# Performance work log

Measured on AMD Instinct MI355X. Metric: run time of the kernel, lower is better.

Reference implementation:

```python
import jax, jax.numpy as jnp
import numpy as np

B, T, DM, H, DH, P = 8, 512, 1024, 16, 64, 3584


def rotate_half(x):
    x1, x2 = x[..., : x.shape[-1] // 2], x[..., x.shape[-1] // 2 :]
    return jnp.concatenate([-x2, x1], axis=-1)


def setup_inputs() -> dict:
    key = jax.random.key(0)
    ks = jax.random.split(key, 16)
    x_new = jax.random.normal(ks[0], (B, T, DM), dtype=jnp.float32)
    # realistic RoPE tables for positions [P, P+T)
    inv_freq = 1.0 / (10000.0 ** (jnp.arange(0, DH, 2, dtype=jnp.float32) / DH))
    pos = jnp.arange(P, P + T, dtype=jnp.float32)
    freqs = pos[:, None] * inv_freq[None, :]  # [T, DH/2]
    emb = jnp.concatenate([freqs, freqs], axis=-1)  # [T, DH]
    rotary_cos = jnp.cos(emb)[None, None]  # [1,1,T,DH]
    rotary_sin = jnp.sin(emb)[None, None]
    past_k = jax.random.normal(ks[1], (B, H, P, DH), dtype=jnp.float32)
    past_v = jax.random.normal(ks[2], (B, H, P, DH), dtype=jnp.float32)
    past_lengths = jax.random.randint(ks[3], (B,), 0, P + 1, dtype=jnp.int32)
    new_token_counts = jax.random.randint(ks[4], (B,), 1, T + 1, dtype=jnp.int32)
    valid_new_mask = jnp.arange(T)[None, :] < new_token_counts[:, None]  # [B,T] bool
    s = 0.02
    Wq = jax.random.normal(ks[5], (DM, DM), dtype=jnp.float32) * s
    Wk = jax.random.normal(ks[6], (DM, DM), dtype=jnp.float32) * s
    Wv = jax.random.normal(ks[7], (DM, DM), dtype=jnp.float32) * s
    Wo = jax.random.normal(ks[8], (DM, DM), dtype=jnp.float32) * s
    bq = jax.random.normal(ks[9], (DM,), dtype=jnp.float32) * s
    bk = jax.random.normal(ks[10], (DM,), dtype=jnp.float32) * s
    bv = jax.random.normal(ks[11], (DM,), dtype=jnp.float32) * s
    bo = jax.random.normal(ks[12], (DM,), dtype=jnp.float32) * s
    return dict(x_new=x_new, rotary_cos=rotary_cos, rotary_sin=rotary_sin,
                past_k=past_k, past_v=past_v, past_lengths=past_lengths,
                valid_new_mask=valid_new_mask, new_token_counts=new_token_counts,
                Wq=Wq, bq=bq, Wk=Wk, bk=bk, Wv=Wv, bv=bv, Wo=Wo, bo=bo)


def reference(x_new, rotary_cos, rotary_sin, past_k, past_v, past_lengths,
              valid_new_mask, new_token_counts, Wq, bq, Wk, bk, Wv, bv, Wo, bo):
    b, t, _ = x_new.shape
    # projections -> [B,H,T,DH]
    def proj(W, bias):
        y = x_new @ W + bias
        return y.reshape(b, t, H, DH).transpose(0, 2, 1, 3)
    q = proj(Wq, bq)
    k_new = proj(Wk, bk)
    v_new = proj(Wv, bv)
    # RoPE on q and new keys
    cos = rotary_cos.astype(q.dtype)
    sin = rotary_sin.astype(q.dtype)
    q = q * cos + rotate_half(q) * sin
    k_new = k_new * cos + rotate_half(k_new) * sin
    # zero out padded new tokens (applied to q, k_new, v_new as in original)
    vmask = valid_new_mask[:, None, :, None].astype(q.dtype)
    q = q * vmask
    k_new = k_new * vmask
    v_new = v_new * vmask
    # trim/mask past cache per sample
    trimmed_past = jnp.clip(past_lengths, 0, P)
    pmask = (jnp.arange(P)[None, :] < trimmed_past[:, None])[:, None, :, None].astype(q.dtype)
    pk = past_k.astype(q.dtype) * pmask
    pv = past_v.astype(q.dtype) * pmask
    k_total = jnp.concatenate([pk, k_new], axis=2)  # [B,H,P+T,DH]
    v_total = jnp.concatenate([pv, v_new], axis=2)
    total_lengths = trimmed_past + new_token_counts  # [B]
    # key validity mask over concatenated axis: positions < total_lengths
    valid_keys = jnp.arange(P + t)[None, :] < total_lengths[:, None]  # [B,S]
    scale = 1.0 / jnp.sqrt(jnp.asarray(DH, dtype=q.dtype))
    scores = jnp.einsum('bhqd,bhkd->bhqk', q, k_total) * scale  # [B,H,T,S]
    neg = jnp.asarray(-1e9, dtype=scores.dtype)
    scores = jnp.where(valid_keys[:, None, None, :], scores, neg)
    attn = jax.nn.softmax(scores, axis=-1)
    out = jnp.einsum('bhqk,bhkd->bhqd', attn, v_total)  # [B,H,T,DH]
    out = out.transpose(0, 2, 1, 3).reshape(b, t, DM)
    out = out @ Wo + bo
    out = out * valid_new_mask[:, :, None].astype(out.dtype)
    return out
```

## Files before the change

kernel.cpp:

```cpp
#include <hip/hip_runtime.h>


typedef unsigned short u16;
typedef unsigned int   u32;
typedef float  f32x4  __attribute__((ext_vector_type(4)));
typedef __bf16 bf16x8 __attribute__((ext_vector_type(8)));

#define DEV static __device__ __forceinline__

constexpr int NP = 3584;

DEV u16 bf16rn(float f){
  u32 u = __float_as_uint(f);
  return (u16)((u + 0x7fffu + ((u >> 16) & 1u)) >> 16);
}
DEV float bf2f(u16 h){ return __uint_as_float((u32)h << 16); }
DEV void split2(float f, u16 &h, u16 &l){ h = bf16rn(f); l = bf16rn(f - bf2f(h)); }

DEV f32x4 mfma16(bf16x8 a, bf16x8 b, f32x4 c){
  return __builtin_amdgcn_mfma_f32_16x16x32_bf16(a, b, c, 0, 0, 0);
}

__global__ __launch_bounds__(256) void k_split_x(const float* __restrict__ x,
                                                 u16* __restrict__ xh, u16* __restrict__ xl){
  int i = blockIdx.x * 256 + threadIdx.x;
  float4 v = ((const float4*)x)[i];
  u16 h0,l0,h1,l1,h2,l2,h3,l3;
  split2(v.x,h0,l0); split2(v.y,h1,l1); split2(v.z,h2,l2); split2(v.w,h3,l3);
  ushort4 hv; hv.x=h0; hv.y=h1; hv.z=h2; hv.w=h3;
  ushort4 lv; lv.x=l0; lv.y=l1; lv.z=l2; lv.w=l3;
  ((ushort4*)xh)[i] = hv; ((ushort4*)xl)[i] = lv;
}

__global__ __launch_bounds__(256) void k_wsplit(const float* __restrict__ w0, const float* __restrict__ w1,
                                                const float* __restrict__ w2, const float* __restrict__ w3,
                                                u16* __restrict__ Wth, u16* __restrict__ Wtl){
  __shared__ float tl[64][65];
  int z = blockIdx.z;
  const float* W = (z==0) ? w0 : (z==1) ? w1 : (z==2) ? w2 : w3;
  u16* oh = Wth + (size_t)z * (1024*1024);
  u16* ol = Wtl + (size_t)z * (1024*1024);
  int n0 = blockIdx.x*64, k0 = blockIdx.y*64;
  int tid = threadIdx.x;
  #pragma unroll
  for (int i=0;i<16;++i){
    int idx = i*256 + tid; int rr = idx >> 6, cc = idx & 63;
    tl[rr][cc] = W[(size_t)(k0+rr)*1024 + n0 + cc];
  }
  __syncthreads();
  #pragma unroll
  for (int i=0;i<16;++i){
    int idx = i*256 + tid; int rr = idx >> 6, cc = idx & 63;
    u16 h,l; split2(tl[cc][rr], h, l);
    size_t o = (size_t)(n0+rr)*1024 + k0 + cc;
    oh[o] = h; ol[o] = l;
  }
}

__global__ __launch_bounds__(256) void k_qkv(
    const u16* __restrict__ xh, const u16* __restrict__ xl,
    const u16* __restrict__ Wth, const u16* __restrict__ Wtl,
    const float* __restrict__ bq, const float* __restrict__ bk, const float* __restrict__ bv,
    const float* __restrict__ rcos, const float* __restrict__ rsin,
    const int* __restrict__ cnts,
    u16* __restrict__ qh, u16* __restrict__ ql,
    u16* __restrict__ kh, u16* __restrict__ vh)
{
  int zi = blockIdx.z;
  int n0 = blockIdx.x * 128, m0 = blockIdx.y * 128;
  int b = m0 >> 9, t0 = m0 & 511;
  int cnt = cnts[b];
  if (t0 >= cnt) return;
  const u16* Bh = Wth + (size_t)zi * (1024*1024);
  const u16* Bl = Wtl + (size_t)zi * (1024*1024);
  const float* bias = (zi==0) ? bq : (zi==1) ? bk : bv;
  u16* oh = (zi==0) ? qh : (zi==1) ? kh : vh;
  u16* ol = ql;

  __shared__ u16 sA[2][128*40];
  __shared__ u16 sB[2][128*40];

  int tid = threadIdx.x, lane = tid & 63, wid = tid >> 6;
  int r = lane & 15, quad = lane >> 4;
  int wm = (wid >> 1) * 64, wn = (wid & 1) * 64;

  const f32x4 fz = {0.f,0.f,0.f,0.f};
  f32x4 acc[4][4];
  #pragma unroll
  for (int i=0;i<4;++i){
    #pragma unroll
    for (int j=0;j<4;++j) acc[i][j] = fz;
  }

  int srow = tid >> 2, sc8 = (tid & 3) * 8;

  for (int kt = 0; kt < 32; ++kt){
    int kb = kt * 32;
    __syncthreads();
    {
      size_t ga  = (size_t)(m0 + srow) * 1024 + kb + sc8;
      size_t gb  = (size_t)(n0 + srow) * 1024 + kb + sc8;
      int lo = srow*40 + sc8, lo2 = lo + 64*40;
      *(uint4*)&sA[0][lo]  = *(const uint4*)&xh[ga];
      *(uint4*)&sA[1][lo]  = *(const uint4*)&xl[ga];
      *(uint4*)&sB[0][lo]  = *(const uint4*)&Bh[gb];
      *(uint4*)&sB[1][lo]  = *(const uint4*)&Bl[gb];
      *(uint4*)&sA[0][lo2] = *(const uint4*)&xh[ga + 64*1024];
      *(uint4*)&sA[1][lo2] = *(const uint4*)&xl[ga + 64*1024];
      *(uint4*)&sB[0][lo2] = *(const uint4*)&Bh[gb + 64*1024];
      *(uint4*)&sB[1][lo2] = *(const uint4*)&Bl[gb + 64*1024];
    }
    __syncthreads();
    bf16x8 ah[4], al[4], bh8[4], bl8[4];
    #pragma unroll
    for (int mf=0; mf<4; ++mf){
      int off = (wm + mf*16 + r)*40 + quad*8;
      ah[mf] = *(const bf16x8*)&sA[0][off];
      al[mf] = *(const bf16x8*)&sA[1][off];
    }
    #pragma unroll
    for (int nf=0; nf<4; ++nf){
      int off = (wn + nf*16 + r)*40 + quad*8;
      bh8[nf] = *(const bf16x8*)&sB[0][off];
      bl8[nf] = *(const bf16x8*)&sB[1][off];
    }
    #pragma unroll
    for (int mf=0; mf<4; ++mf){
      #pragma unroll
      for (int nf=0; nf<4; ++nf){
        acc[mf][nf] = mfma16(ah[mf], bh8[nf], acc[mf][nf]);
        acc[mf][nf] = mfma16(al[mf], bh8[nf], acc[mf][nf]);
        acc[mf][nf] = mfma16(ah[mf], bl8[nf], acc[mf][nf]);
      }
    }
  }

  float vals[4][4][4];
  #pragma unroll
  for (int mf=0;mf<4;++mf){
    #pragma unroll
    for (int nf=0;nf<4;++nf){
      float bb = bias[n0 + wn + nf*16 + r];
      #pragma unroll
      for (int e=0;e<4;++e) vals[mf][nf][e] = acc[mf][nf][e] + bb;
    }
  }
  if (zi < 2){
    #pragma unroll
    for (int mf=0;mf<4;++mf){
      #pragma unroll
      for (int e=0;e<4;++e){
        int t = t0 + wm + mf*16 + quad*4 + e;
        #pragma unroll
        for (int nf=0;nf<2;++nf){
          int d = nf*16 + r;
          float c1 = rcos[t*64 + d],      s1 = rsin[t*64 + d];
          float c2 = rcos[t*64 + d + 32], s2 = rsin[t*64 + d + 32];
          float x1 = vals[mf][nf][e], x2 = vals[mf][nf+2][e];
          vals[mf][nf][e]   = x1*c1 - x2*s1;
          vals[mf][nf+2][e] = x2*c2 + x1*s2;
        }
      }
    }
  }
  #pragma unroll
  for (int mf=0;mf<4;++mf){
    #pragma unroll
    for (int e=0;e<4;++e){
      int t = t0 + wm + mf*16 + quad*4 + e;
      float msk = (t < cnt) ? 1.f : 0.f;
      #pragma unroll
      for (int nf=0;nf<4;++nf){
        int gc = n0 + wn + nf*16 + r;
        int head = gc >> 6, d = gc & 63;
        float v = vals[mf][nf][e] * msk;
        u16 hh, ll; split2(v, hh, ll);
        size_t o = ((size_t)(b*16 + head)*512 + t)*64 + d;
        oh[o] = hh;
        if (zi == 0) ol[o] = ll;
      }
    }
  }
}

__global__ __launch_bounds__(256,3) void k_attn(
    const u16* __restrict__ qh_, const u16* __restrict__ ql_,
    const u16* __restrict__ knh, const u16* __restrict__ vnh,
    const float* __restrict__ pk, const float* __restrict__ pv,
    const int* __restrict__ plen, const int* __restrict__ cnts,
    int S, float* __restrict__ pl, float* __restrict__ pO)
{
  int qt = blockIdx.x, h = blockIdx.y;
  int zb = blockIdx.z;
  int b = zb / S, s = zb - b * S;
  int cnt = cnts[b];
  int q0 = qt * 128;
  if (q0 >= cnt) return;
  int Lp = min(max(plen[b], 0), NP);
  int TL = Lp + cnt;
  int Ln = max(0, TL - NP);
  int jend = min(((Lp + 63) >> 6) << 6, NP);
  int minTLP = min(TL, NP);
  int Zar = max(0, minTLP - jend);
  int npast = jend >> 6, nnew = (Ln + 63) >> 6;
  int Tt = npast + nnew;
  int qsp = (Tt + S - 1) / S;
  int it0 = s * qsp, it1 = min(Tt, it0 + qsp);
  bool hasZ = (s == 0 && Zar > 0);
  if (it0 >= it1 && !hasZ) return;

  __shared__ u16 sK [64*72];
  __shared__ u16 sVT[64*72];
  __shared__ u16 sP [4*32*72];

  int tid = threadIdx.x, lane = tid & 63, wid = tid >> 6;
  int r = lane & 15, quad = lane >> 4;
  int wm0 = wid * 32;

  bf16x8 Qh[2][2], Ql[2][2];
  size_t qbase = ((size_t)(b*16 + h)*512 + q0 + wm0) * 64;
  #pragma unroll
  for (int mf=0;mf<2;++mf){
    #pragma unroll
    for (int ks=0;ks<2;++ks){
      size_t o = qbase + (size_t)(mf*16 + r)*64 + ks*32 + quad*8;
      Qh[mf][ks] = *(const bf16x8*)&qh_[o];
      Ql[mf][ks] = *(const bf16x8*)&ql_[o];
    }
  }

  const f32x4 fz = {0.f,0.f,0.f,0.f};
  f32x4 O[2][4];
  float lsum[2][4];
  #pragma unroll
  for (int mf=0;mf<2;++mf){
    #pragma unroll
    for (int e=0;e<4;++e) lsum[mf][e] = 0.f;
    #pragma unroll
    for (int nf=0;nf<4;++nf) O[mf][nf] = fz;
  }

  const float kscale = 0.125f * 1.44269504088896340736f;
  size_t kvb = (size_t)(b*16 + h) * NP  * 64;
  size_t nb  = (size_t)(b*16 + h) * 512 * 64;
  int sj = tid >> 4, sd0 = (tid & 15) * 4;

  float4 kbuf[4];
  bool nisp = false; int nj0 = 0;
  auto issueK = [&](int itn){
    nisp = itn < npast;
    nj0 = (nisp ? itn : itn - npast) << 6;
    if (nisp){
      #pragma unroll
      for (int i=0;i<4;++i){
        int j = sj + i*16;
        kbuf[i] = *(const float4*)&pk[kvb + (size_t)(nj0 + j)*64 + sd0];
      }
    } else {
      #pragma unroll
      for (int i=0;i<2;++i){
        int j = (tid>>3) + i*32, d0 = (tid & 7)*8;
        kbuf[i] = *(const float4*)&knh[nb + (size_t)(nj0 + j)*64 + d0];
      }
    }
  };
  if (it0 < it1) issueK(it0);

  for (int it = it0; it < it1; ++it){
    bool ispc = nisp; int j0c = nj0;

    if (ispc){
      #pragma unroll
      for (int i=0;i<4;++i){
        int j = sj + i*16;
        float4 kv = kbuf[i];
        if (j0c + j >= Lp){ kv.x=0.f; kv.y=0.f; kv.z=0.f; kv.w=0.f; }
        ushort4 khv; khv.x=bf16rn(kv.x); khv.y=bf16rn(kv.y); khv.z=bf16rn(kv.z); khv.w=bf16rn(kv.w);
        *(ushort4*)&sK[j*72 + sd0] = khv;
      }
    } else {
      #pragma unroll
      for (int i=0;i<2;++i){
        int j = (tid>>3) + i*32, d0 = (tid & 7)*8;
        *(uint4*)&sK[j*72 + d0] = __builtin_bit_cast(uint4, kbuf[i]);
      }
    }

    float4  pvv[4];
    ushort4 vnr[4];
    if (ispc){
      #pragma unroll
      for (int i=0;i<4;++i){
        int j = sj + i*16;
        pvv[i] = *(const float4*)&pv[kvb + (size_t)(j0c + j)*64 + sd0];
      }
    } else {
      #pragma unroll
      for (int i=0;i<4;++i){
        int j = sj + i*16;
        vnr[i] = *(const ushort4*)&vnh[nb + (size_t)(j0c + j)*64 + sd0];
      }
    }

    if (it + 1 < it1) issueK(it + 1);

    __syncthreads();

    f32x4 Sc[2][4];
    #pragma unroll
    for (int mf=0;mf<2;++mf){
      #pragma unroll
      for (int jf=0;jf<4;++jf) Sc[mf][jf] = fz;
    }
    #pragma unroll
    for (int ks=0;ks<2;++ks){
      #pragma unroll
      for (int jf=0;jf<4;++jf){
        int off = (jf*16 + r)*72 + ks*32 + quad*8;
        bf16x8 kbh = *(const bf16x8*)&sK[off];
        #pragma unroll
        for (int mf=0;mf<2;++mf){
          Sc[mf][jf] = mfma16(Qh[mf][ks], kbh, Sc[mf][jf]);
          Sc[mf][jf] = mfma16(Ql[mf][ks], kbh, Sc[mf][jf]);
        }
      }
    }

    if (ispc){
      #pragma unroll
      for (int i=0;i<4;++i){
        int j = sj + i*16;
        float4 vv = pvv[i];
        if (j0c + j >= Lp){ vv.x=0.f; vv.y=0.f; vv.z=0.f; vv.w=0.f; }
        sVT[(sd0+0)*72 + j] = bf16rn(vv.x);
        sVT[(sd0+1)*72 + j] = bf16rn(vv.y);
        sVT[(sd0+2)*72 + j] = bf16rn(vv.z);
        sVT[(sd0+3)*72 + j] = bf16rn(vv.w);
      }
    } else {
      #pragma unroll
      for (int i=0;i<4;++i){
        int j = sj + i*16;
        sVT[(sd0+0)*72 + j] = vnr[i].x;
        sVT[(sd0+1)*72 + j] = vnr[i].y;
        sVT[(sd0+2)*72 + j] = vnr[i].z;
        sVT[(sd0+3)*72 + j] = vnr[i].w;
      }
    }

    int jlim = (ispc ? TL : Ln) - j0c;
    #pragma unroll
    for (int mf=0;mf<2;++mf){
      #pragma unroll
      for (int e=0;e<4;++e){
        int pbase = wid*2304 + (mf*16 + quad*4 + e)*72;
        float ls = 0.f;
        #pragma unroll
        for (int jf=0;jf<4;++jf){
          float sv = Sc[mf][jf][e] * kscale - 4.0f;
          sv = (jf*16 + r < jlim) ? sv : -3.0e38f;
          float pj = exp2f(sv);
          ls += pj;
          sP[pbase + jf*16 + r] = bf16rn(pj);
        }
        lsum[mf][e] += ls;
      }
    }
    __syncthreads();

    #pragma unroll
    for (int ks=0;ks<2;++ks){
      bf16x8 pah[2];
      #pragma unroll
      for (int mf=0;mf<2;++mf){
        int off = wid*2304 + (mf*16 + r)*72 + ks*32 + quad*8;
        pah[mf] = *(const bf16x8*)&sP[off];
      }
      #pragma unroll
      for (int nf=0;nf<4;++nf){
        int off = (nf*16 + r)*72 + ks*32 + quad*8;
        bf16x8 vbh = *(const bf16x8*)&sVT[off];
        #pragma unroll
        for (int mf=0;mf<2;++mf){
          O[mf][nf] = mfma16(pah[mf], vbh, O[mf][nf]);
        }
      }
    }
  }

  int pidx = ((b*16 + h)*4 + qt)*S + s;
  float* plr = pl + (size_t)pidx*128;
  float* po  = pO + (size_t)pidx*8192;
  float zadd = (s == 0) ? (float)Zar * 0.0625f : 0.f;
  #pragma unroll
  for (int mf=0;mf<2;++mf){
    #pragma unroll
    for (int e=0;e<4;++e){
      int row = wm0 + mf*16 + quad*4 + e;
      float l = lsum[mf][e];
      l += __shfl_xor(l, 1);
      l += __shfl_xor(l, 2);
      l += __shfl_xor(l, 4);
      l += __shfl_xor(l, 8);
      if (r == 0) plr[row] = l + zadd;
      #pragma unroll
      for (int nf=0;nf<4;++nf) po[row*64 + nf*16 + r] = O[mf][nf][e];
    }
  }
}

__global__ __launch_bounds__(256) void k_reduce(
    const float* __restrict__ pl, const float* __restrict__ pO,
    const int* __restrict__ plen, const int* __restrict__ cnts,
    int S, u16* __restrict__ aoh, u16* __restrict__ aol)
{
  int qt = blockIdx.x, h = blockIdx.y, b = blockIdx.z;
  int cnt = cnts[b]; int q0 = qt*128;
  if (q0 >= cnt) return;
  int Lp = min(max(plen[b], 0), NP);
  int TL = Lp + cnt;
  int Ln = max(0, TL - NP);
  int jend = min(((Lp + 63) >> 6) << 6, NP);
  int minTLP = min(TL, NP);
  int Zar = max(0, minTLP - jend);
  int npast = jend >> 6, nnew = (Ln + 63) >> 6;
  int Tt = npast + nnew;
  int qsp = (Tt + S - 1) / S;

  int tid = threadIdx.x;
  int row = tid >> 1, c0 = (tid & 1) * 32;
  int base = ((b*16 + h)*4 + qt)*S;

  float L = 0.f;
  float acc[32];
  #pragma unroll
  for (int i=0;i<32;++i) acc[i] = 0.f;
  for (int s2=0;s2<S;++s2){
    bool act = (s2*qsp < Tt) || (s2 == 0 && Zar > 0);
    if (!act) continue;
    L += pl[(size_t)(base+s2)*128 + row];
    const float4* po = (const float4*)(pO + (size_t)(base+s2)*8192 + row*64 + c0);
    #pragma unroll
    for (int i=0;i<8;++i){
      float4 v = po[i];
      acc[4*i+0] += v.x; acc[4*i+1] += v.y; acc[4*i+2] += v.z; acc[4*i+3] += v.w;
    }
  }
  float inv = 1.f / L;
  size_t o = ((size_t)b*512 + q0 + row)*1024 + h*64 + c0;
  #pragma unroll
  for (int i=0;i<8;++i){
    ushort4 hv, lv;
    u16 hh, ll;
    split2(acc[4*i+0]*inv, hh, ll); hv.x=hh; lv.x=ll;
    split2(acc[4*i+1]*inv, hh, ll); hv.y=hh; lv.y=ll;
    split2(acc[4*i+2]*inv, hh, ll); hv.z=hh; lv.z=ll;
    split2(acc[4*i+3]*inv, hh, ll); hv.w=hh; lv.w=ll;
    *(ushort4*)&aoh[o + 4*i] = hv;
    *(ushort4*)&aol[o + 4*i] = lv;
  }
}

__global__ __launch_bounds__(256) void k_oproj(
    const u16* __restrict__ ah_, const u16* __restrict__ al_,
    const u16* __restrict__ Wth, const u16* __restrict__ Wtl,
    const float* __restrict__ bo, const int* __restrict__ cnts,
    float* __restrict__ out)
{
  int n0 = blockIdx.x * 128, m0 = blockIdx.y * 128;
  int b = m0 >> 9, t0 = m0 & 511;
  int cnt = cnts[b];
  int tid = threadIdx.x;
  if (t0 >= cnt){
    float4 z4 = {0.f,0.f,0.f,0.f};
    #pragma unroll
    for (int i=0;i<16;++i){
      int v = tid + i*256;
      int row = v >> 5, c4 = (v & 31) * 4;
      *(float4*)&out[(size_t)(m0+row)*1024 + n0 + c4] = z4;
    }
    return;
  }
  const u16* Bh = Wth + 3ull*1024*1024;
  const u16* Bl = Wtl + 3ull*1024*1024;

  __shared__ u16 sA[2][128*40];
  __shared__ u16 sB[2][128*40];

  int lane = tid & 63, wid = tid >> 6;
  int r = lane & 15, quad = lane >> 4;
  int wm = (wid >> 1) * 64, wn = (wid & 1) * 64;

  const f32x4 fz = {0.f,0.f,0.f,0.f};
  f32x4 acc[4][4];
  #pragma unroll
  for (int i=0;i<4;++i){
    #pragma unroll
    for (int j=0;j<4;++j) acc[i][j] = fz;
  }

  int srow = tid >> 2, sc8 = (tid & 3) * 8;

  for (int kt = 0; kt < 32; ++kt){
    int kb = kt * 32;
    __syncthreads();
    {
      size_t ga  = (size_t)(m0 + srow) * 1024 + kb + sc8;
      size_t gb  = (size_t)(n0 + srow) * 1024 + kb + sc8;
      int lo = srow*40 + sc8, lo2 = lo + 64*40;
      *(uint4*)&sA[0][lo]  = *(const uint4*)&ah_[ga];
      *(uint4*)&sA[1][lo]  = *(const uint4*)&al_[ga];
      *(uint4*)&sB[0][lo]  = *(const uint4*)&Bh[gb];
      *(uint4*)&sB[1][lo]  = *(const uint4*)&Bl[gb];
      *(uint4*)&sA[0][lo2] = *(const uint4*)&ah_[ga + 64*1024];
      *(uint4*)&sA[1][lo2] = *(const uint4*)&al_[ga + 64*1024];
      *(uint4*)&sB[0][lo2] = *(const uint4*)&Bh[gb + 64*1024];
      *(uint4*)&sB[1][lo2] = *(const uint4*)&Bl[gb + 64*1024];
    }
    __syncthreads();
    bf16x8 ah8[4], al8[4], bh8[4], bl8[4];
    #pragma unroll
    for (int mf=0; mf<4; ++mf){
      int off = (wm + mf*16 + r)*40 + quad*8;
      ah8[mf] = *(const bf16x8*)&sA[0][off];
      al8[mf] = *(const bf16x8*)&sA[1][off];
    }
    #pragma unroll
    for (int nf=0; nf<4; ++nf){
      int off = (wn + nf*16 + r)*40 + quad*8;
      bh8[nf] = *(const bf16x8*)&sB[0][off];
      bl8[nf] = *(const bf16x8*)&sB[1][off];
    }
    #pragma unroll
    for (int mf=0; mf<4; ++mf){
      #pragma unroll
      for (int nf=0; nf<4; ++nf){
        acc[mf][nf] = mfma16(ah8[mf], bh8[nf], acc[mf][nf]);
        acc[mf][nf] = mfma16(al8[mf], bh8[nf], acc[mf][nf]);
        acc[mf][nf] = mfma16(ah8[mf], bl8[nf], acc[mf][nf]);
      }
    }
  }

  #pragma unroll
  for (int mf=0;mf<4;++mf){
    #pragma unroll
    for (int e=0;e<4;++e){
      int t = t0 + wm + mf*16 + quad*4 + e;
      float msk = (t < cnt) ? 1.f : 0.f;
      int row = m0 + wm + mf*16 + quad*4 + e;
      #pragma unroll
      for (int nf=0;nf<4;++nf){
        int gc = n0 + wn + nf*16 + r;
        out[(size_t)row*1024 + gc] = (acc[mf][nf][e] + bo[gc]) * msk;
      }
    }
  }
}

extern "C" void kernel_launch(void* const* d_in, const int* in_sizes, int n_in,
                              void* d_out, int out_size, void* d_ws, size_t ws_size,
                              hipStream_t stream) {
  (void)in_sizes; (void)n_in; (void)out_size;
  const float* x    = (const float*)d_in[0];
  const float* rcos = (const float*)d_in[1];
  const float* rsin = (const float*)d_in[2];
  const float* pk   = (const float*)d_in[3];
  const float* pv   = (const float*)d_in[4];
  const int*   plen = (const int*)d_in[5];
  const int*   cnts = (const int*)d_in[7];
  const float* Wq = (const float*)d_in[8];
  const float* bq = (const float*)d_in[9];
  const float* Wk = (const float*)d_in[10];
  const float* bk = (const float*)d_in[11];
  const float* Wv = (const float*)d_in[12];
  const float* bv = (const float*)d_in[13];
  const float* Wo = (const float*)d_in[14];
  const float* bo = (const float*)d_in[15];
  float* out = (float*)d_out;

  char* w = (char*)d_ws;
  const size_t SLOT = 8ull * 1024 * 1024;
  u16* xh  = (u16*)(w + 0*SLOT);
  u16* xl  = (u16*)(w + 1*SLOT);
  u16* Wth = (u16*)(w + 2*SLOT);
  u16* Wtl = (u16*)(w + 3*SLOT);
  u16* qh  = (u16*)(w + 4*SLOT);
  u16* ql  = (u16*)(w + 5*SLOT);
  u16* knh = (u16*)(w + 6*SLOT);
  u16* vnh = (u16*)(w + 7*SLOT);
  float* pl = (float*)(w + 8*SLOT);
  float* pO = (float*)(w + 8*SLOT + (2ull<<20));
  u16* aoh = xh;
  u16* aol = xl;

  size_t used = 8*SLOT + (2ull<<20);
  int S = (int)((ws_size - used) / (16ull<<20));
  if (S > 8) S = 8;
  if (S < 1) S = 1;

  k_split_x<<<dim3(4096), dim3(256), 0, stream>>>(x, xh, xl);
  k_wsplit<<<dim3(16,16,4), dim3(256), 0, stream>>>(Wq, Wk, Wv, Wo, Wth, Wtl);
  k_qkv<<<dim3(8,32,3), dim3(256), 0, stream>>>(xh, xl, Wth, Wtl, bq, bk, bv,
                                                rcos, rsin, cnts,
                                                qh, ql, knh, vnh);
  k_attn<<<dim3(4,16,8*S), dim3(256), 0, stream>>>(qh, ql, knh, vnh,
                                                   pk, pv, plen, cnts, S, pl, pO);
  k_reduce<<<dim3(4,16,8), dim3(256), 0, stream>>>(pl, pO, plen, cnts, S, aoh, aol);
  k_oproj<<<dim3(8,32), dim3(256), 0, stream>>>(aoh, aol, Wth, Wtl, bo, cnts, out);
}
```

Measured before the change: 589.3 us.

## Reorder V loads, swizzle LDS P/V tiles, use non-draining barriers and setprio

V loads for the current tile are issued before the K staging so they have more time in flight. The V transpose store moves after the softmax, so it overlaps with exp work. __syncthreads is replaced by a barrier that waits only on LDS counters, which lets outstanding global prefetches stay in flight across it. An XOR swizzle on the sP and sVT layouts targets LDS bank conflicts, and s_setprio raises wave priority around the MFMA blocks. The non-draining barrier relies on the prefetched registers not being consumed before their vmcnt is satisfied, which the compiler must still ensure.

```diff
diff --git a/kernel.cpp b/kernel.cpp
--- a/kernel.cpp
+++ b/kernel.cpp
@@ -20,6 +20,14 @@
 DEV f32x4 mfma16(bf16x8 a, bf16x8 b, f32x4 c){
   return __builtin_amdgcn_mfma_f32_16x16x32_bf16(a, b, c, 0, 0, 0);
 }
+
+DEV void bar_nodrain(){
+  asm volatile("s_waitcnt lgkmcnt(0)" ::: "memory");
+  __builtin_amdgcn_s_barrier();
+  __builtin_amdgcn_sched_barrier(0);
+}
+
+DEV int swz(int row, int col){ return col ^ (((row >> 2) & 7) << 3); }
 
 __global__ __launch_bounds__(256) void k_split_x(const float* __restrict__ x,
                                                  u16* __restrict__ xh, u16* __restrict__ xl){
@@ -269,6 +277,22 @@
   for (int it = it0; it < it1; ++it){
     bool ispc = nisp; int j0c = nj0;
 
+    float4  pvv[4];
+    ushort4 vnr[4];
+    if (ispc){
+      #pragma unroll
+      for (int i=0;i<4;++i){
+        int j = sj + i*16;
+        pvv[i] = *(const float4*)&pv[kvb + (size_t)(j0c + j)*64 + sd0];
+      }
+    } else {
+      #pragma unroll
+      for (int i=0;i<4;++i){
+        int j = sj + i*16;
+        vnr[i] = *(const ushort4*)&vnh[nb + (size_t)(j0c + j)*64 + sd0];
+      }
+    }
+
     if (ispc){
       #pragma unroll
       for (int i=0;i<4;++i){
@@ -286,25 +310,9 @@
       }
     }
 
-    float4  pvv[4];
-    ushort4 vnr[4];
-    if (ispc){
-      #pragma unroll
-      for (int i=0;i<4;++i){
-        int j = sj + i*16;
-        pvv[i] = *(const float4*)&pv[kvb + (size_t)(j0c + j)*64 + sd0];
-      }
-    } else {
-      #pragma unroll
-      for (int i=0;i<4;++i){
-        int j = sj + i*16;
-        vnr[i] = *(const ushort4*)&vnh[nb + (size_t)(j0c + j)*64 + sd0];
-      }
-    }
-
     if (it + 1 < it1) issueK(it + 1);
 
-    __syncthreads();
+    bar_nodrain();
 
     f32x4 Sc[2][4];
     #pragma unroll
@@ -312,6 +320,7 @@
       #pragma unroll
       for (int jf=0;jf<4;++jf) Sc[mf][jf] = fz;
     }
+    __builtin_amdgcn_s_setprio(1);
     #pragma unroll
     for (int ks=0;ks<2;++ks){
       #pragma unroll
@@ -325,35 +334,15 @@
         }
       }
     }
-
-    if (ispc){
-      #pragma unroll
-      for (int i=0;i<4;++i){
-        int j = sj + i*16;
-        float4 vv = pvv[i];
-        if (j0c + j >= Lp){ vv.x=0.f; vv.y=0.f; vv.z=0.f; vv.w=0.f; }
-        sVT[(sd0+0)*72 + j] = bf16rn(vv.x);
-        sVT[(sd0+1)*72 + j] = bf16rn(vv.y);
-        sVT[(sd0+2)*72 + j] = bf16rn(vv.z);
-        sVT[(sd0+3)*72 + j] = bf16rn(vv.w);
-      }
-    } else {
-      #pragma unroll
-      for (int i=0;i<4;++i){
-        int j = sj + i*16;
-        sVT[(sd0+0)*72 + j] = vnr[i].x;
-        sVT[(sd0+1)*72 + j] = vnr[i].y;
-        sVT[(sd0+2)*72 + j] = vnr[i].z;
-        sVT[(sd0+3)*72 + j] = vnr[i].w;
-      }
-    }
+    __builtin_amdgcn_s_setprio(0);
 
     int jlim = (ispc ? TL : Ln) - j0c;
     #pragma unroll
     for (int mf=0;mf<2;++mf){
       #pragma unroll
       for (int e=0;e<4;++e){
-        int pbase = wid*2304 + (mf*16 + quad*4 + e)*72;
+        int row = mf*16 + quad*4 + e;
+        int pbase = wid*2304 + row*72;
         float ls = 0.f;
         #pragma unroll
         for (int jf=0;jf<4;++jf){
@@ -361,31 +350,56 @@
           sv = (jf*16 + r < jlim) ? sv : -3.0e38f;
           float pj = exp2f(sv);
           ls += pj;
-          sP[pbase + jf*16 + r] = bf16rn(pj);
+          sP[pbase + swz(row, jf*16 + r)] = bf16rn(pj);
         }
         lsum[mf][e] += ls;
       }
     }
-    __syncthreads();
-
+
+    if (ispc){
+      #pragma unroll
+      for (int i=0;i<4;++i){
+        int j = sj + i*16;
+        float4 vv = pvv[i];
+        if (j0c + j >= Lp){ vv.x=0.f; vv.y=0.f; vv.z=0.f; vv.w=0.f; }
+        sVT[(sd0+0)*72 + swz(sd0+0, j)] = bf16rn(vv.x);
+        sVT[(sd0+1)*72 + swz(sd0+1, j)] = bf16rn(vv.y);
+        sVT[(sd0+2)*72 + swz(sd0+2, j)] = bf16rn(vv.z);
+        sVT[(sd0+3)*72 + swz(sd0+3, j)] = bf16rn(vv.w);
+      }
+    } else {
+      #pragma unroll
+      for (int i=0;i<4;++i){
+        int j = sj + i*16;
+        sVT[(sd0+0)*72 + swz(sd0+0, j)] = vnr[i].x;
+        sVT[(sd0+1)*72 + swz(sd0+1, j)] = vnr[i].y;
+        sVT[(sd0+2)*72 + swz(sd0+2, j)] = vnr[i].z;
+        sVT[(sd0+3)*72 + swz(sd0+3, j)] = vnr[i].w;
+      }
+    }
+
+    bar_nodrain();
+
+    __builtin_amdgcn_s_setprio(1);
     #pragma unroll
     for (int ks=0;ks<2;++ks){
       bf16x8 pah[2];
       #pragma unroll
       for (int mf=0;mf<2;++mf){
-        int off = wid*2304 + (mf*16 + r)*72 + ks*32 + quad*8;
-        pah[mf] = *(const bf16x8*)&sP[off];
+        int row = mf*16 + r;
+        pah[mf] = *(const bf16x8*)&sP[wid*2304 + row*72 + swz(row, ks*32 + quad*8)];
       }
       #pragma unroll
       for (int nf=0;nf<4;++nf){
-        int off = (nf*16 + r)*72 + ks*32 + quad*8;
-        bf16x8 vbh = *(const bf16x8*)&sVT[off];
+        int row = nf*16 + r;
+        bf16x8 vbh = *(const bf16x8*)&sVT[row*72 + swz(row, ks*32 + quad*8)];
         #pragma unroll
         for (int mf=0;mf<2;++mf){
           O[mf][nf] = mfma16(pah[mf], vbh, O[mf][nf]);
         }
       }
     }
+    __builtin_amdgcn_s_setprio(0);
   }
 
   int pidx = ((b*16 + h)*4 + qt)*S + s;
```

Result: slower. 731.7 us (+24.2%).

## Pre-convert past KV to swizzled bf16 and stage tiles via async global-to-LDS loads

Applied to the files above, without the earlier changes.

Adds a k_conv pass that converts the fp32 past K/V cache to bf16 once, zero-masks entries beyond each sample's past length, and writes K row-major and V transposed, both XOR-swizzled. The QKV projection now writes new K/V in the same tiled, swizzled layout. The attention kernel then loads K/V tiles with global_load_lds into double-buffered LDS, with swizzled reads replacing the padded layouts. This removes the repeated fp32 loads, per-tile conversion and transposed scalar LDS stores from the attention inner loop. The cost is an extra conversion kernel, more workspace, and reuse of the x buffers for the converted cache.

```diff
diff --git a/kernel.cpp b/kernel.cpp
--- a/kernel.cpp
+++ b/kernel.cpp
@@ -19,6 +19,15 @@
 
 DEV f32x4 mfma16(bf16x8 a, bf16x8 b, f32x4 c){
   return __builtin_amdgcn_mfma_f32_16x16x32_bf16(a, b, c, 0, 0, 0);
+}
+
+DEV ushort4 cvt4(float4 v){
+  ushort4 h; h.x=bf16rn(v.x); h.y=bf16rn(v.y); h.z=bf16rn(v.z); h.w=bf16rn(v.w); return h;
+}
+
+DEV void gload_lds16(const u16* g, u16* l){
+  __builtin_amdgcn_global_load_lds((const __attribute__((address_space(1))) void*)g,
+                                   (__attribute__((address_space(3))) void*)l, 16, 0, 0);
 }
 
 __global__ __launch_bounds__(256) void k_split_x(const float* __restrict__ x,
@@ -64,7 +73,7 @@
     const float* __restrict__ rcos, const float* __restrict__ rsin,
     const int* __restrict__ cnts,
     u16* __restrict__ qh, u16* __restrict__ ql,
-    u16* __restrict__ kh, u16* __restrict__ vh)
+    u16* __restrict__ knt, u16* __restrict__ vnt)
 {
   int zi = blockIdx.z;
   int n0 = blockIdx.x * 128, m0 = blockIdx.y * 128;
@@ -74,8 +83,6 @@
   const u16* Bh = Wth + (size_t)zi * (1024*1024);
   const u16* Bl = Wtl + (size_t)zi * (1024*1024);
   const float* bias = (zi==0) ? bq : (zi==1) ? bk : bv;
-  u16* oh = (zi==0) ? qh : (zi==1) ? kh : vh;
-  u16* ol = ql;
 
   __shared__ u16 sA[2][128*40];
   __shared__ u16 sB[2][128*40];
@@ -175,18 +182,82 @@
         int head = gc >> 6, d = gc & 63;
         float v = vals[mf][nf][e] * msk;
         u16 hh, ll; split2(v, hh, ll);
-        size_t o = ((size_t)(b*16 + head)*512 + t)*64 + d;
-        oh[o] = hh;
-        if (zi == 0) ol[o] = ll;
-      }
-    }
+        size_t bh8t = (size_t)(b*16 + head)*8;
+        if (zi == 0){
+          size_t o = ((size_t)(b*16 + head)*512 + t)*64 + d;
+          qh[o] = hh; ql[o] = ll;
+        } else if (zi == 1){
+          size_t o = ((bh8t + (t>>6))*64 + (t&63))*64 + (d ^ ((t&7)<<3));
+          knt[o] = hh;
+        } else {
+          size_t o = ((bh8t + (t>>6))*64 + d)*64 + ((t&63) ^ ((d&7)<<3));
+          vnt[o] = hh;
+        }
+      }
+    }
+  }
+}
+
+__global__ __launch_bounds__(256) void k_conv(
+    const float* __restrict__ pk, const float* __restrict__ pv,
+    const int* __restrict__ plen,
+    u16* __restrict__ ckh, u16* __restrict__ cvt)
+{
+  int t = blockIdx.x, h = blockIdx.y, b = blockIdx.z;
+  int Lp = min(max(plen[b], 0), NP);
+  int jend = min(((Lp + 63) >> 6) << 6, NP);
+  if (t*64 >= jend) return;
+  int tid = threadIdx.x;
+  int bh = b*16 + h;
+  int row = tid >> 2, cg = (tid & 3) * 16;
+  int jj = t*64 + row;
+  size_t src = ((size_t)bh*NP + jj)*64;
+
+  __shared__ float tl[64][65];
+
+  float4 kv4[4], vv4[4];
+  #pragma unroll
+  for (int i=0;i<4;++i){
+    kv4[i] = *(const float4*)&pk[src + cg + i*4];
+    vv4[i] = *(const float4*)&pv[src + cg + i*4];
+  }
+  if (jj >= Lp){
+    float4 z4 = {0.f,0.f,0.f,0.f};
+    #pragma unroll
+    for (int i=0;i<4;++i){ kv4[i]=z4; vv4[i]=z4; }
+  }
+  size_t kdst = ((size_t)bh*NP + jj)*64;
+  #pragma unroll
+  for (int i=0;i<4;++i){
+    int c4 = cg + i*4;
+    *(ushort4*)&ckh[kdst + (c4 ^ ((jj&7)<<3))] = cvt4(kv4[i]);
+  }
+  #pragma unroll
+  for (int i=0;i<4;++i){
+    tl[row][cg+i*4+0] = vv4[i].x;
+    tl[row][cg+i*4+1] = vv4[i].y;
+    tl[row][cg+i*4+2] = vv4[i].z;
+    tl[row][cg+i*4+3] = vv4[i].w;
+  }
+  __syncthreads();
+  int d = tid >> 2, jg = (tid & 3) * 16;
+  size_t vdst = (((size_t)bh*56 + t)*64 + d)*64;
+  #pragma unroll
+  for (int i=0;i<4;++i){
+    int j4 = jg + i*4;
+    ushort4 hv;
+    hv.x = bf16rn(tl[j4+0][d]);
+    hv.y = bf16rn(tl[j4+1][d]);
+    hv.z = bf16rn(tl[j4+2][d]);
+    hv.w = bf16rn(tl[j4+3][d]);
+    *(ushort4*)&cvt[vdst + (j4 ^ ((d&7)<<3))] = hv;
   }
 }
 
 __global__ __launch_bounds__(256,3) void k_attn(
     const u16* __restrict__ qh_, const u16* __restrict__ ql_,
-    const u16* __restrict__ knh, const u16* __restrict__ vnh,
-    const float* __restrict__ pk, const float* __restrict__ pv,
+    const u16* __restrict__ knt, const u16* __restrict__ vnt,
+    const u16* __restrict__ ckh, const u16* __restrict__ cvt,
     const int* __restrict__ plen, const int* __restrict__ cnts,
     int S, float* __restrict__ pl, float* __restrict__ pO)
 {
@@ -204,21 +275,23 @@
   int Zar = max(0, minTLP - jend);
   int npast = jend >> 6, nnew = (Ln + 63) >> 6;
   int Tt = npast + nnew;
+  int TLu = min(TL, jend) + Ln;
   int qsp = (Tt + S - 1) / S;
   int it0 = s * qsp, it1 = min(Tt, it0 + qsp);
   bool hasZ = (s == 0 && Zar > 0);
   if (it0 >= it1 && !hasZ) return;
 
-  __shared__ u16 sK [64*72];
-  __shared__ u16 sVT[64*72];
-  __shared__ u16 sP [4*32*72];
+  __shared__ __align__(16) u16 sK [2][4096];
+  __shared__ __align__(16) u16 sVT[2][4096];
+  __shared__ __align__(16) u16 sP [4][2048];
 
   int tid = threadIdx.x, lane = tid & 63, wid = tid >> 6;
   int r = lane & 15, quad = lane >> 4;
   int wm0 = wid * 32;
+  int bh = b*16 + h;
 
   bf16x8 Qh[2][2], Ql[2][2];
-  size_t qbase = ((size_t)(b*16 + h)*512 + q0 + wm0) * 64;
+  size_t qbase = ((size_t)bh*512 + q0 + wm0) * 64;
   #pragma unroll
   for (int mf=0;mf<2;++mf){
     #pragma unroll
@@ -241,70 +314,29 @@
   }
 
   const float kscale = 0.125f * 1.44269504088896340736f;
-  size_t kvb = (size_t)(b*16 + h) * NP  * 64;
-  size_t nb  = (size_t)(b*16 + h) * 512 * 64;
-  int sj = tid >> 4, sd0 = (tid & 15) * 4;
-
-  float4 kbuf[4];
-  bool nisp = false; int nj0 = 0;
-  auto issueK = [&](int itn){
-    nisp = itn < npast;
-    nj0 = (nisp ? itn : itn - npast) << 6;
-    if (nisp){
-      #pragma unroll
-      for (int i=0;i<4;++i){
-        int j = sj + i*16;
-        kbuf[i] = *(const float4*)&pk[kvb + (size_t)(nj0 + j)*64 + sd0];
-      }
+  int ub = wid * 512;
+
+  auto stage = [&](int pp, int it){
+    const u16* ks; const u16* vs;
+    if (it < npast){
+      ks = ckh + ((size_t)bh*NP + (size_t)it*64)*64;
+      vs = cvt + ((size_t)bh*56 + it)*4096;
     } else {
-      #pragma unroll
-      for (int i=0;i<2;++i){
-        int j = (tid>>3) + i*32, d0 = (tid & 7)*8;
-        kbuf[i] = *(const float4*)&knh[nb + (size_t)(nj0 + j)*64 + d0];
-      }
-    }
+      ks = knt + ((size_t)bh*8 + (it - npast))*4096;
+      vs = vnt + ((size_t)bh*8 + (it - npast))*4096;
+    }
+    gload_lds16(ks + ub + lane*8,        &sK [pp][ub]);
+    gload_lds16(ks + ub + 2048 + lane*8, &sK [pp][ub + 2048]);
+    gload_lds16(vs + ub + lane*8,        &sVT[pp][ub]);
+    gload_lds16(vs + ub + 2048 + lane*8, &sVT[pp][ub + 2048]);
   };
-  if (it0 < it1) issueK(it0);
+
+  int p = 0;
+  if (it0 < it1) stage(0, it0);
+  __syncthreads();
 
   for (int it = it0; it < it1; ++it){
-    bool ispc = nisp; int j0c = nj0;
-
-    if (ispc){
-      #pragma unroll
-      for (int i=0;i<4;++i){
-        int j = sj + i*16;
-        float4 kv = kbuf[i];
-        if (j0c + j >= Lp){ kv.x=0.f; kv.y=0.f; kv.z=0.f; kv.w=0.f; }
-        ushort4 khv; khv.x=bf16rn(kv.x); khv.y=bf16rn(kv.y); khv.z=bf16rn(kv.z); khv.w=bf16rn(kv.w);
-        *(ushort4*)&sK[j*72 + sd0] = khv;
-      }
-    } else {
-      #pragma unroll
-      for (int i=0;i<2;++i){
-        int j = (tid>>3) + i*32, d0 = (tid & 7)*8;
-        *(uint4*)&sK[j*72 + d0] = __builtin_bit_cast(uint4, kbuf[i]);
-      }
-    }
-
-    float4  pvv[4];
-    ushort4 vnr[4];
-    if (ispc){
-      #pragma unroll
-      for (int i=0;i<4;++i){
-        int j = sj + i*16;
-        pvv[i] = *(const float4*)&pv[kvb + (size_t)(j0c + j)*64 + sd0];
-      }
-    } else {
-      #pragma unroll
-      for (int i=0;i<4;++i){
-        int j = sj + i*16;
-        vnr[i] = *(const ushort4*)&vnh[nb + (size_t)(j0c + j)*64 + sd0];
-      }
-    }
-
-    if (it + 1 < it1) issueK(it + 1);
-
-    __syncthreads();
+    if (it + 1 < it1) stage(p^1, it + 1);
 
     f32x4 Sc[2][4];
     #pragma unroll
@@ -316,8 +348,9 @@
     for (int ks=0;ks<2;++ks){
       #pragma unroll
       for (int jf=0;jf<4;++jf){
-        int off = (jf*16 + r)*72 + ks*32 + quad*8;
-        bf16x8 kbh = *(const bf16x8*)&sK[off];
+        int jr = jf*16 + r;
+        int off = jr*64 + ((ks*32 + quad*8) ^ ((jr&7)<<3));
+        bf16x8 kbh = *(const bf16x8*)&sK[p][off];
         #pragma unroll
         for (int mf=0;mf<2;++mf){
           Sc[mf][jf] = mfma16(Qh[mf][ks], kbh, Sc[mf][jf]);
@@ -326,34 +359,13 @@
       }
     }
 
-    if (ispc){
-      #pragma unroll
-      for (int i=0;i<4;++i){
-        int j = sj + i*16;
-        float4 vv = pvv[i];
-        if (j0c + j >= Lp){ vv.x=0.f; vv.y=0.f; vv.z=0.f; vv.w=0.f; }
-        sVT[(sd0+0)*72 + j] = bf16rn(vv.x);
-        sVT[(sd0+1)*72 + j] = bf16rn(vv.y);
-        sVT[(sd0+2)*72 + j] = bf16rn(vv.z);
-        sVT[(sd0+3)*72 + j] = bf16rn(vv.w);
-      }
-    } else {
-      #pragma unroll
-      for (int i=0;i<4;++i){
-        int j = sj + i*16;
-        sVT[(sd0+0)*72 + j] = vnr[i].x;
-        sVT[(sd0+1)*72 + j] = vnr[i].y;
-        sVT[(sd0+2)*72 + j] = vnr[i].z;
-        sVT[(sd0+3)*72 + j] = vnr[i].w;
-      }
-    }
-
-    int jlim = (ispc ? TL : Ln) - j0c;
+    int jlim = TLu - it*64;
     #pragma unroll
     for (int mf=0;mf<2;++mf){
       #pragma unroll
       for (int e=0;e<4;++e){
-        int pbase = wid*2304 + (mf*16 + quad*4 + e)*72;
+        int row = mf*16 + quad*4 + e;
+        int sw = ((row>>2)&7) << 3;
         float ls = 0.f;
         #pragma unroll
         for (int jf=0;jf<4;++jf){
@@ -361,7 +373,8 @@
           sv = (jf*16 + r < jlim) ? sv : -3.0e38f;
           float pj = exp2f(sv);
           ls += pj;
-          sP[pbase + jf*16 + r] = bf16rn(pj);
+          __bf16 pb = (__bf16)pj;
+          sP[wid][row*64 + ((jf*16 + r) ^ sw)] = __builtin_bit_cast(u16, pb);
         }
         lsum[mf][e] += ls;
       }
@@ -373,19 +386,21 @@
       bf16x8 pah[2];
       #pragma unroll
       for (int mf=0;mf<2;++mf){
-        int off = wid*2304 + (mf*16 + r)*72 + ks*32 + quad*8;
-        pah[mf] = *(const bf16x8*)&sP[off];
+        int row = mf*16 + r;
+        pah[mf] = *(const bf16x8*)&sP[wid][row*64 + ((ks*32 + quad*8) ^ (((row>>2)&7)<<3))];
       }
       #pragma unroll
       for (int nf=0;nf<4;++nf){
-        int off = (nf*16 + r)*72 + ks*32 + quad*8;
-        bf16x8 vbh = *(const bf16x8*)&sVT[off];
+        int d = nf*16 + r;
+        bf16x8 vbh = *(const bf16x8*)&sVT[p][d*64 + ((ks*32 + quad*8) ^ ((d&7)<<3))];
         #pragma unroll
         for (int mf=0;mf<2;++mf){
           O[mf][nf] = mfma16(pah[mf], vbh, O[mf][nf]);
         }
       }
     }
+    __syncthreads();
+    p ^= 1;
   }
 
   int pidx = ((b*16 + h)*4 + qt)*S + s;
@@ -580,22 +595,23 @@
   float* out = (float*)d_out;
 
   char* w = (char*)d_ws;
-  const size_t SLOT = 8ull * 1024 * 1024;
-  u16* xh  = (u16*)(w + 0*SLOT);
-  u16* xl  = (u16*)(w + 1*SLOT);
-  u16* Wth = (u16*)(w + 2*SLOT);
-  u16* Wtl = (u16*)(w + 3*SLOT);
-  u16* qh  = (u16*)(w + 4*SLOT);
-  u16* ql  = (u16*)(w + 5*SLOT);
-  u16* knh = (u16*)(w + 6*SLOT);
-  u16* vnh = (u16*)(w + 7*SLOT);
-  float* pl = (float*)(w + 8*SLOT);
-  float* pO = (float*)(w + 8*SLOT + (2ull<<20));
+  const size_t MB = 1ull << 20;
+  u16* Wth = (u16*)(w + 0*MB);
+  u16* Wtl = (u16*)(w + 8*MB);
+  u16* qh  = (u16*)(w + 16*MB);
+  u16* ql  = (u16*)(w + 24*MB);
+  u16* knt = (u16*)(w + 32*MB);
+  u16* vnt = (u16*)(w + 40*MB);
+  u16* ckh = (u16*)(w + 48*MB);
+  u16* xh  = (u16*)(w + 48*MB);
+  u16* xl  = (u16*)(w + 56*MB);
+  u16* cvt = (u16*)(w + 104*MB);
+  float* pl = (float*)(w + 160*MB);
+  float* pO = (float*)(w + 162*MB);
   u16* aoh = xh;
   u16* aol = xl;
 
-  size_t used = 8*SLOT + (2ull<<20);
-  int S = (int)((ws_size - used) / (16ull<<20));
+  int S = (int)((ws_size - 162*MB) / (16*MB));
   if (S > 8) S = 8;
   if (S < 1) S = 1;
 
@@ -603,9 +619,10 @@
   k_wsplit<<<dim3(16,16,4), dim3(256), 0, stream>>>(Wq, Wk, Wv, Wo, Wth, Wtl);
   k_qkv<<<dim3(8,32,3), dim3(256), 0, stream>>>(xh, xl, Wth, Wtl, bq, bk, bv,
                                                 rcos, rsin, cnts,
-                                                qh, ql, knh, vnh);
-  k_attn<<<dim3(4,16,8*S), dim3(256), 0, stream>>>(qh, ql, knh, vnh,
-                                                   pk, pv, plen, cnts, S, pl, pO);
+                                                qh, ql, knt, vnt);
+  k_conv<<<dim3(56,16,8), dim3(256), 0, stream>>>(pk, pv, plen, ckh, cvt);
+  k_attn<<<dim3(4,16,8*S), dim3(256), 0, stream>>>(qh, ql, knt, vnt, ckh, cvt,
+                                                   plen, cnts, S, pl, pO);
   k_reduce<<<dim3(4,16,8), dim3(256), 0, stream>>>(pl, pO, plen, cnts, S, aoh, aol);
   k_oproj<<<dim3(8,32), dim3(256), 0, stream>>>(aoh, aol, Wth, Wtl, bo, cnts, out);
 }
```

Result: no change. 583.5 us (-1.0%).
